# Kernel optimization log

Hardware: AMD Instinct MI355X
Metric: run time of the kernel (lower is better)

The kernel has to match this reference:

```python
import jax, jax.numpy as jnp
import numpy as np

B, S, D_IN = 4, 4096, 4096
G, R, GROUP_DIM = 8, 256, 512  # num_groups, rank per group, out_features // num_groups


def setup_inputs() -> dict:
    key = jax.random.key(0)
    k1, k2, k3 = jax.random.split(key, 3)
    scale = 1.0 / np.sqrt(D_IN)
    hidden_states = jax.random.normal(k1, (B, S, D_IN), dtype=jnp.float32)
    VT_w = jax.random.normal(k2, (G * R, D_IN), dtype=jnp.float32) * scale  # nn.Linear weight layout (out, in)
    U_w = jax.random.normal(k3, (G, GROUP_DIM, R), dtype=jnp.float32) * (1.0 / np.sqrt(R))  # per-group Linear weights
    return {"hidden_states": hidden_states, "VT_w": VT_w, "U_w": U_w}


def reference(hidden_states, VT_w, U_w):
    # shared low-rank down-projection: (B,S,D_in) @ VT_w.T -> (B,S,G*R)
    latent = jnp.einsum('bsd,rd->bsr', hidden_states, VT_w)
    # since all ranks are equal, the per-group loop + concat is a block-diagonal GEMM:
    latent = latent.reshape(B, S, G, R)
    out = jnp.einsum('bsgr,gor->bsgo', latent, U_w)  # per-group up-projection (o = group_dim)
    return out.reshape(B, S, G * GROUP_DIM)
```

## Files before the change

kernel.cpp:

```cpp
#include <hip/hip_runtime.h>
#include <stdint.h>


typedef short  bf16x8  __attribute__((ext_vector_type(8)));
typedef float  f32x4   __attribute__((ext_vector_type(4)));
typedef ushort ushort8 __attribute__((ext_vector_type(8)));
typedef float  flt4    __attribute__((ext_vector_type(4)));

__device__ __forceinline__ void gload_lds16(const ushort* g, ushort* l) {
    __builtin_amdgcn_global_load_lds(
        (const __attribute__((address_space(1))) uint32_t*)g,
        (__attribute__((address_space(3))) uint32_t*)l, 16, 0, 0);
}

__device__ __forceinline__ ushort f2bf(float f) {
    union { float f; uint32_t u; } c; c.f = f;
    uint32_t u = c.u;
    uint32_t r = (u + 0x7FFFu + ((u >> 16) & 1u)) >> 16;
    return (ushort)r;
}

__device__ __forceinline__ void conv_seg(const float* __restrict__ in,
                                         ushort* __restrict__ out,
                                         long n8, int bid, int nblk) {
    const long stride = (long)nblk * 256;
    for (long i = (long)bid * 256 + threadIdx.x; i < n8; i += stride) {
        flt4 a = ((const flt4*)in)[2 * i];
        flt4 b = ((const flt4*)in)[2 * i + 1];
        ushort8 o;
        o[0] = f2bf(a[0]); o[1] = f2bf(a[1]); o[2] = f2bf(a[2]); o[3] = f2bf(a[3]);
        o[4] = f2bf(b[0]); o[5] = f2bf(b[1]); o[6] = f2bf(b[2]); o[7] = f2bf(b[3]);
        ((ushort8*)out)[i] = o;
    }
}

__global__ __launch_bounds__(256) void convert_all_kernel(
    const float* __restrict__ hid_f, ushort* __restrict__ hid_b, long nHid8,
    const float* __restrict__ vt_f,  ushort* __restrict__ vt_b,  long nVT8,
    const float* __restrict__ u_f,   ushort* __restrict__ u_b,   long nU8)
{
    const int b = blockIdx.x;
    if (b < 1792)      conv_seg(hid_f, hid_b, nHid8, b,        1792);
    else if (b < 2016) conv_seg(vt_f,  vt_b,  nVT8,  b - 1792, 224);
    else               conv_seg(u_f,   u_b,   nU8,   b - 2016, 32);
}

__device__ __forceinline__ void store_out(ushort* p, float v) { *p = f2bf(v); }
__device__ __forceinline__ void store_out(float*  p, float v) { *p = v; }

template <typename TOUT>
__global__ __launch_bounds__(512) void gemm_bt_kernel(
    const ushort* __restrict__ A,
    const ushort* __restrict__ B,
    TOUT* __restrict__ C,
    int lda, int ldb, int ldc, int K, int bxShift,
    long aOffZ, long bOffZ, long cOffZ)
{
    A += (size_t)blockIdx.z * aOffZ;
    B += (size_t)blockIdx.z * bOffZ;
    C += (size_t)blockIdx.z * cOffZ;

    __shared__ ushort As[128 * 64];
    __shared__ ushort Bs[128 * 64];

    const int tid  = threadIdx.x;
    const int lane = tid & 63;
    const int wave = tid >> 6;

    const int bid = blockIdx.x;
    const int xcd = bid & 7;
    const int rr  = bid >> 3;
    const int by  = xcd * 16 + (rr >> bxShift);
    const int bx  = rr & ((1 << bxShift) - 1);

    const int row0 = by * 128;
    const int col0 = bx * 128;

    const int wr = wave >> 2;
    const int wc = wave & 3;

    const int l15    = lane & 15;
    const int lq     = lane >> 4;
    const int lrow   = lane >> 3;
    const int lchunk = lane & 7;

    f32x4 acc[4][2] = {};

    const ushort* aPtr = A + (size_t)(row0 + wave * 8 + lrow) * lda + lchunk * 8;
    const ushort* bPtr = B + (size_t)(col0 + wave * 8 + lrow) * ldb + lchunk * 8;
    const int ldsseg = wave * 512;

    const int nkt = K / 64;
    for (int kt = 0; kt < nkt; ++kt) {
        const int kOff = kt * 64;
        __syncthreads();
        #pragma unroll
        for (int i = 0; i < 2; ++i) {
            gload_lds16(aPtr + (size_t)i * 64 * lda + kOff, As + i * 4096 + ldsseg);
            gload_lds16(bPtr + (size_t)i * 64 * ldb + kOff, Bs + i * 4096 + ldsseg);
        }
        __syncthreads();

        #pragma unroll
        for (int kk = 0; kk < 2; ++kk) {
            bf16x8 af[4], bfr[2];
            #pragma unroll
            for (int m = 0; m < 4; ++m)
                af[m] = *(const bf16x8*)&As[(wr * 64 + m * 16 + l15) * 64 + kk * 32 + lq * 8];
            #pragma unroll
            for (int n = 0; n < 2; ++n)
                bfr[n] = *(const bf16x8*)&Bs[(wc * 32 + n * 16 + l15) * 64 + kk * 32 + lq * 8];
            #pragma unroll
            for (int m = 0; m < 4; ++m)
                #pragma unroll
                for (int n = 0; n < 2; ++n)
                    acc[m][n] = __builtin_amdgcn_mfma_f32_16x16x32_bf16(
                        af[m], bfr[n], acc[m][n], 0, 0, 0);
        }
    }

    #pragma unroll
    for (int m = 0; m < 4; ++m) {
        #pragma unroll
        for (int r = 0; r < 4; ++r) {
            const size_t row = (size_t)(row0 + wr * 64 + m * 16 + lq * 4 + r);
            TOUT* cRow = C + row * ldc + col0 + wc * 32 + l15;
            #pragma unroll
            for (int n = 0; n < 2; ++n)
                store_out(cRow + n * 16, acc[m][n][r]);
        }
    }
}

extern "C" void kernel_launch(void* const* d_in, const int* in_sizes, int n_in,
                              void* d_out, int out_size, void* d_ws, size_t ws_size,
                              hipStream_t stream) {
    const float* hidden_f = (const float*)d_in[0];
    const float* VT_f     = (const float*)d_in[1];
    const float* U_f      = (const float*)d_in[2];
    float* out = (float*)d_out;

    const long nHid = 16384L * 4096L;
    const long nVT  = 2048L * 4096L;
    const long nU   = 8L * 512L * 256L;
    const long nLat = 16384L * 2048L;

    ushort *hid_b, *vt_b, *u_b, *lat_b;
    const size_t needA = (size_t)(nHid + nVT + nU + nLat) * 2;
    if (ws_size >= needA) {
        ushort* w = (ushort*)d_ws;
        hid_b = w;  vt_b = hid_b + nHid;  u_b = vt_b + nVT;  lat_b = u_b + nU;
    } else {
        ushort* w = (ushort*)d_ws;
        lat_b = w;  u_b = lat_b + nLat;
        ushort* o = (ushort*)d_out;
        hid_b = o;  vt_b = hid_b + nHid;
    }

    convert_all_kernel<<<dim3(2048), dim3(256), 0, stream>>>(
        hidden_f, hid_b, nHid / 8,
        VT_f,     vt_b,  nVT / 8,
        U_f,      u_b,   nU / 8);

    gemm_bt_kernel<ushort><<<dim3(2048, 1, 1), dim3(512), 0, stream>>>(
        hid_b, vt_b, lat_b, 4096, 4096, 2048, 4096, 4,
        0L, 0L, 0L);

    gemm_bt_kernel<float><<<dim3(512, 1, 8), dim3(512), 0, stream>>>(
        lat_b, u_b, out, 2048, 256, 4096, 256, 2,
        256L, 512L * 256L, 512L);
}
```

Measured before the change: 572.6 us.

## Fuse fp32-to-bf16 conversion of hidden states into first GEMM's A-tile load

Removes the separate conversion pass over the 256MB fp32 hidden_states. The first GEMM now reads fp32 directly, converts it with v_cvt_pk_bf16_f32 and writes bf16 into LDS through registers. Only VT and U are still converted in a standalone kernel. The first GEMM also moves from 512 threads to 256 threads, each wave holding a 64x64 sub-tile. This avoids writing the bf16 copy and reading it back, but the A loads become register round-trips instead of direct-to-LDS loads, which may expose latency because nothing is double-buffered.

```diff
diff --git a/kernel.cpp b/kernel.cpp
--- a/kernel.cpp
+++ b/kernel.cpp
@@ -18,6 +18,12 @@
     uint32_t u = c.u;
     uint32_t r = (u + 0x7FFFu + ((u >> 16) & 1u)) >> 16;
     return (ushort)r;
+}
+
+__device__ __forceinline__ uint32_t cvtpk(float lo, float hi) {
+    uint32_t r;
+    asm("v_cvt_pk_bf16_f32 %0, %1, %2" : "=v"(r) : "v"(lo), "v"(hi));
+    return r;
 }
 
 __device__ __forceinline__ void conv_seg(const float* __restrict__ in,
@@ -34,22 +40,108 @@
     }
 }
 
-__global__ __launch_bounds__(256) void convert_all_kernel(
-    const float* __restrict__ hid_f, ushort* __restrict__ hid_b, long nHid8,
-    const float* __restrict__ vt_f,  ushort* __restrict__ vt_b,  long nVT8,
-    const float* __restrict__ u_f,   ushort* __restrict__ u_b,   long nU8)
+__global__ __launch_bounds__(256) void convert_vt_u_kernel(
+    const float* __restrict__ vt_f, ushort* __restrict__ vt_b, long nVT8,
+    const float* __restrict__ u_f,  ushort* __restrict__ u_b,  long nU8)
 {
     const int b = blockIdx.x;
-    if (b < 1792)      conv_seg(hid_f, hid_b, nHid8, b,        1792);
-    else if (b < 2016) conv_seg(vt_f,  vt_b,  nVT8,  b - 1792, 224);
-    else               conv_seg(u_f,   u_b,   nU8,   b - 2016, 32);
+    if (b < 896) conv_seg(vt_f, vt_b, nVT8, b,       896);
+    else         conv_seg(u_f,  u_b,  nU8,  b - 896, 128);
 }
 
 __device__ __forceinline__ void store_out(ushort* p, float v) { *p = f2bf(v); }
 __device__ __forceinline__ void store_out(float*  p, float v) { *p = v; }
 
+__global__ __launch_bounds__(256) void gemm1_fused_kernel(
+    const float* __restrict__ Af,
+    const ushort* __restrict__ B,
+    ushort* __restrict__ C,
+    int lda, int ldb, int ldc, int K, int bxShift)
+{
+    __shared__ ushort As[128 * 64];
+    __shared__ ushort Bs[128 * 64];
+
+    const int tid  = threadIdx.x;
+    const int lane = tid & 63;
+    const int wave = tid >> 6;
+
+    const int bid = blockIdx.x;
+    const int xcd = bid & 7;
+    const int rr  = bid >> 3;
+    const int by  = xcd * 16 + (rr >> bxShift);
+    const int bx  = rr & ((1 << bxShift) - 1);
+
+    const int row0 = by * 128;
+    const int col0 = bx * 128;
+
+    const int wr = wave >> 1;
+    const int wc = wave & 1;
+
+    const int l15    = lane & 15;
+    const int lq     = lane >> 4;
+    const int lrow   = lane >> 3;
+    const int lchunk = lane & 7;
+
+    f32x4 acc[4][4] = {};
+
+    const float*  aF   = Af + (size_t)(row0 + wave * 32 + lrow) * lda + lchunk * 8;
+    const ushort* bPtr = B  + (size_t)(col0 + wave * 32 + lrow) * ldb + lchunk * 8;
+    ushort* aDstBase = As + wave * 4 * 512 + lane * 8;
+
+    const int nkt = K / 64;
+    for (int kt = 0; kt < nkt; ++kt) {
+        const int kOff = kt * 64;
+        __syncthreads();
+        #pragma unroll
+        for (int i = 0; i < 4; ++i)
+            gload_lds16(bPtr + (size_t)i * 8 * ldb + kOff, Bs + (wave * 4 + i) * 512);
+        #pragma unroll
+        for (int i = 0; i < 4; ++i) {
+            const float* src = aF + (size_t)(i * 8) * lda + kOff;
+            flt4 lo = *(const flt4*)(src);
+            flt4 hi = *(const flt4*)(src + 4);
+            uint4 w;
+            w.x = cvtpk(lo[0], lo[1]);
+            w.y = cvtpk(lo[2], lo[3]);
+            w.z = cvtpk(hi[0], hi[1]);
+            w.w = cvtpk(hi[2], hi[3]);
+            *(uint4*)(aDstBase + i * 512) = w;
+        }
+        __syncthreads();
+
+        #pragma unroll
+        for (int kk = 0; kk < 2; ++kk) {
+            bf16x8 af[4], bfr[4];
+            #pragma unroll
+            for (int m = 0; m < 4; ++m)
+                af[m] = *(const bf16x8*)&As[(wr * 64 + m * 16 + l15) * 64 + kk * 32 + lq * 8];
+            #pragma unroll
+            for (int n = 0; n < 4; ++n)
+                bfr[n] = *(const bf16x8*)&Bs[(wc * 64 + n * 16 + l15) * 64 + kk * 32 + lq * 8];
+            #pragma unroll
+            for (int m = 0; m < 4; ++m)
+                #pragma unroll
+                for (int n = 0; n < 4; ++n)
+                    acc[m][n] = __builtin_amdgcn_mfma_f32_16x16x32_bf16(
+                        af[m], bfr[n], acc[m][n], 0, 0, 0);
+        }
+    }
+
+    #pragma unroll
+    for (int m = 0; m < 4; ++m) {
+        #pragma unroll
+        for (int r = 0; r < 4; ++r) {
+            const size_t row = (size_t)(row0 + wr * 64 + m * 16 + lq * 4 + r);
+            ushort* cRow = C + row * ldc + col0 + wc * 64 + l15;
+            #pragma unroll
+            for (int n = 0; n < 4; ++n)
+                cRow[n * 16] = f2bf(acc[m][n][r]);
+        }
+    }
+}
+
 template <typename TOUT>
-__global__ __launch_bounds__(512) void gemm_bt_kernel(
+__global__ __launch_bounds__(512) void gemm_bt8_kernel(
     const ushort* __restrict__ A,
     const ushort* __restrict__ B,
     TOUT* __restrict__ C,
@@ -140,33 +232,24 @@
     const float* U_f      = (const float*)d_in[2];
     float* out = (float*)d_out;
 
-    const long nHid = 16384L * 4096L;
     const long nVT  = 2048L * 4096L;
     const long nU   = 8L * 512L * 256L;
     const long nLat = 16384L * 2048L;
 
-    ushort *hid_b, *vt_b, *u_b, *lat_b;
-    const size_t needA = (size_t)(nHid + nVT + nU + nLat) * 2;
-    if (ws_size >= needA) {
-        ushort* w = (ushort*)d_ws;
-        hid_b = w;  vt_b = hid_b + nHid;  u_b = vt_b + nVT;  lat_b = u_b + nU;
-    } else {
-        ushort* w = (ushort*)d_ws;
-        lat_b = w;  u_b = lat_b + nLat;
-        ushort* o = (ushort*)d_out;
-        hid_b = o;  vt_b = hid_b + nHid;
-    }
-
-    convert_all_kernel<<<dim3(2048), dim3(256), 0, stream>>>(
-        hidden_f, hid_b, nHid / 8,
-        VT_f,     vt_b,  nVT / 8,
-        U_f,      u_b,   nU / 8);
-
-    gemm_bt_kernel<ushort><<<dim3(2048, 1, 1), dim3(512), 0, stream>>>(
-        hid_b, vt_b, lat_b, 4096, 4096, 2048, 4096, 4,
-        0L, 0L, 0L);
-
-    gemm_bt_kernel<float><<<dim3(512, 1, 8), dim3(512), 0, stream>>>(
+    ushort *vt_b, *u_b, *lat_b;
+    const size_t needA = (size_t)(nVT + nU + nLat) * 2;
+    ushort* w = (ushort*)d_ws;
+    lat_b = w;  u_b = lat_b + nLat;
+    if (ws_size >= needA) vt_b = u_b + nU;
+    else                  vt_b = (ushort*)d_out;
+
+    convert_vt_u_kernel<<<dim3(1024), dim3(256), 0, stream>>>(
+        VT_f, vt_b, nVT / 8, U_f, u_b, nU / 8);
+
+    gemm1_fused_kernel<<<dim3(2048, 1, 1), dim3(256), 0, stream>>>(
+        hidden_f, vt_b, lat_b, 4096, 4096, 2048, 4096, 4);
+
+    gemm_bt8_kernel<float><<<dim3(512, 1, 8), dim3(512), 0, stream>>>(
         lat_b, u_b, out, 2048, 256, 4096, 256, 2,
         256L, 512L * 256L, 512L);
 }
```

New measurement: 533.3 us. 6.9% less time.
